# Kernel tuning notes

Hardware: AMD Instinct MI355X
Metric: run time of the kernel (lower is better)

The kernel has to match this reference:

```python
import jax, jax.numpy as jnp
import numpy as np

N_NODES = 60000
N_EDGES = 300000
FACE_DIM = 32
EDGE_DIM = 16
GF = 64   # EGAT node/edge hidden dim
EF = 32   # NNConv output dim
FF = 32   # placeholder point-transformer dim (zeros path)
TOT = GF + EF + FF  # 128
NEG_SLOPE = 0.01    # torch LeakyReLU default inside DGL EGATConv


def _leaky(x):
    return jnp.where(x >= 0, x, NEG_SLOPE * x)


def _edge_softmax(logits, dst, n):
    # softmax over incoming edges of each destination node (DGL edge_softmax)
    m = jax.ops.segment_max(logits, dst, num_segments=n)
    e = jnp.exp(logits - m[dst])
    s = jax.ops.segment_sum(e, dst, num_segments=n)
    return e / s[dst]


def _egat(h, f, src, dst, n, w_ni, w_nj, w_fij, w_node, attn, bias):
    # DGL EGATConv with num_heads=1 (head dim squeezed)
    f_out = _leaky((h @ w_ni)[src] + (h @ w_nj)[dst] + f @ w_fij + bias)  # (E, GF)
    a = _edge_softmax(f_out @ attn, dst, n)                               # (E,)
    msg = (h @ w_node)[src] * a[:, None]                                  # (E, GF)
    h_out = jax.ops.segment_sum(msg, dst, num_segments=n)                 # (N, GF)
    return h_out, f_out


def setup_inputs() -> dict:
    key = jax.random.key(0)
    ks = iter(jax.random.split(key, 40))

    def w(shape, scale=0.1):
        return jax.random.normal(next(ks), shape, dtype=jnp.float32) * scale

    inp = {
        "face_features": jax.random.normal(next(ks), (N_NODES, FACE_DIM), dtype=jnp.float32),
        "edge_features": jax.random.normal(next(ks), (N_EDGES, EDGE_DIM), dtype=jnp.float32),
        "fp_w": w((FACE_DIM, GF)), "fp_b": w((GF,)),
        "ep_w": w((EDGE_DIM, GF)), "ep_b": w((GF,)),
        "nn_w": w((EDGE_DIM, FACE_DIM * EF), 0.05), "nn_b": w((FACE_DIM * EF,), 0.05),
        "nn_bias": w((EF,)),
        "gate_w": w((TOT, 1)), "gate_b": w((1,)),
        "src": jax.random.randint(next(ks), (N_EDGES,), 0, N_NODES),
        "dst": jax.random.randint(next(ks), (N_EDGES,), 0, N_NODES),
    }
    for L in ("e1", "e2"):
        inp[f"{L}_ni"] = w((GF, GF))
        inp[f"{L}_nj"] = w((GF, GF))
        inp[f"{L}_fij"] = w((GF, GF))
        inp[f"{L}_node"] = w((GF, GF))
        inp[f"{L}_attn"] = w((GF,))
        inp[f"{L}_bias"] = w((GF,))
    return inp


def reference(face_features, edge_features, fp_w, fp_b, ep_w, ep_b,
              nn_w, nn_b, nn_bias, gate_w, gate_b,
              e1_ni, e1_nj, e1_fij, e1_node, e1_attn, e1_bias,
              e2_ni, e2_nj, e2_fij, e2_node, e2_attn, e2_bias,
              src, dst):
    n = face_features.shape[0]
    # --- Gf: two stacked EGATConv layers on projected features ---
    h = face_features @ fp_w + fp_b
    f = edge_features @ ep_w + ep_b
    h, f = _egat(h, f, src, dst, n, e1_ni, e1_nj, e1_fij, e1_node, e1_attn, e1_bias)
    h, f = _egat(h, f, src, dst, n, e2_ni, e2_nj, e2_fij, e2_node, e2_attn, e2_bias)
    Gf = h
    # --- Ef: NNConv (edge-conditioned conv, mean aggregation) ---
    W_e = (edge_features @ nn_w + nn_b).reshape(-1, FACE_DIM, EF)      # (E, 32, 32)
    m = jnp.einsum('ei,eio->eo', face_features[src], W_e)              # (E, EF)
    s = jax.ops.segment_sum(m, dst, num_segments=n)
    cnt = jax.ops.segment_sum(jnp.ones((m.shape[0],), m.dtype), dst, num_segments=n)
    Ef_feat = s / jnp.maximum(cnt, 1.0)[:, None] + nn_bias             # (N, EF)
    # --- Ff: zeros (face_point_features=None path) ---
    Ff_feat = jnp.zeros((n, FF), dtype=Gf.dtype)
    node_features = jnp.concatenate([Gf, Ef_feat, Ff_feat], axis=-1)   # (N, 128)
    # --- GlobalAttentionPooling (single graph) ---
    gate = jax.nn.softmax(node_features @ gate_w + gate_b, axis=0)     # (N, 1)
    graph_feat = jnp.sum(gate * node_features, axis=0, keepdims=True)  # (1, 128)
    return node_features, graph_feat
```

## Files before the change

### kernel.cpp

```cpp
#include <hip/hip_runtime.h>

#define NN 60000
#define NE 300000
#define PB 768
typedef unsigned short ush;
typedef __attribute__((ext_vector_type(8))) short bf16x8;
typedef __attribute__((ext_vector_type(4))) float f32x4;

static inline int cdiv(int a, int b) { return (a + b - 1) / b; }

__device__ inline unsigned ord_enc(float x) {
  unsigned u = __float_as_uint(x);
  return (u & 0x80000000u) ? ~u : (u | 0x80000000u);
}
__device__ inline float ord_dec(unsigned u) {
  return __uint_as_float((u & 0x80000000u) ? (u & 0x7fffffffu) : ~u);
}
__device__ inline float bf2f(unsigned u16) { return __uint_as_float(u16 << 16); }
__device__ inline ush f2bf(float x) {
  unsigned u = __float_as_uint(x);
  return (ush)((u + 0x7FFFu + ((u >> 16) & 1u)) >> 16);
}
__device__ inline unsigned pack2(float lo, float hi) {
  return ((unsigned)f2bf(hi) << 16) | (unsigned)f2bf(lo);
}

__global__ void deg_kernel(const int* __restrict__ key, int* __restrict__ deg) {
  int e = blockIdx.x * blockDim.x + threadIdx.x;
  if (e < NE) atomicAdd(deg + key[e], 1);
}

__global__ void scan1_kernel(const int* __restrict__ deg, int* __restrict__ rowptr,
                             int* __restrict__ partial) {
  __shared__ int s[256];
  int i = blockIdx.x * 256 + threadIdx.x;
  int v = (i < NN) ? deg[i] : 0;
  s[threadIdx.x] = v;
  __syncthreads();
  for (int off = 1; off < 256; off <<= 1) {
    int t = (threadIdx.x >= off) ? s[threadIdx.x - off] : 0;
    __syncthreads();
    s[threadIdx.x] += t;
    __syncthreads();
  }
  if (i < NN) rowptr[i] = s[threadIdx.x] - v;
  if (threadIdx.x == 255) partial[blockIdx.x] = s[255];
}

__global__ void scan2_kernel(int* __restrict__ partial, int nb) {
  __shared__ int s[256];
  int v = (threadIdx.x < nb) ? partial[threadIdx.x] : 0;
  s[threadIdx.x] = v;
  __syncthreads();
  for (int off = 1; off < 256; off <<= 1) {
    int t = (threadIdx.x >= off) ? s[threadIdx.x - off] : 0;
    __syncthreads();
    s[threadIdx.x] += t;
    __syncthreads();
  }
  if (threadIdx.x < nb) partial[threadIdx.x] = s[threadIdx.x] - v;
}

__global__ void scan3_kernel(int* __restrict__ rowptr, const int* __restrict__ partial,
                             int* __restrict__ cursor) {
  int i = blockIdx.x * 256 + threadIdx.x;
  if (i < NN) {
    int r = rowptr[i] + partial[blockIdx.x];
    rowptr[i] = r;
    cursor[i] = r;
  }
}

__global__ void scatter_dst_kernel(const int* __restrict__ src, const int* __restrict__ dst,
                                   const float* __restrict__ ef, int* __restrict__ cursor,
                                   int* __restrict__ src_s, int* __restrict__ dst_s,
                                   ush* __restrict__ ef16) {
  int e = blockIdx.x * blockDim.x + threadIdx.x;
  if (e >= NE) return;
  int d = dst[e];
  int j = atomicAdd(cursor + d, 1);
  src_s[j] = src[e];
  dst_s[j] = d;
  const float4* ep = (const float4*)(ef + (size_t)e * 16);
  float4 a = ep[0], b = ep[1], c = ep[2], dd = ep[3];
  uint4* bp = (uint4*)(ef16 + (size_t)j * 32);
  uint4 p0, p1;
  p0.x = pack2(a.x, a.y); p0.y = pack2(a.z, a.w);
  p0.z = pack2(b.x, b.y); p0.w = pack2(b.z, b.w);
  p1.x = pack2(c.x, c.y); p1.y = pack2(c.z, c.w);
  p1.z = pack2(dd.x, dd.y); p1.w = pack2(dd.z, dd.w);
  bp[0] = p0; bp[1] = p1;
  bp[2] = make_uint4(0, 0, 0, 0);
  bp[3] = make_uint4(0, 0, 0, 0);
}

__global__ void face16_kernel(const float* __restrict__ face, ush* __restrict__ face16) {
  int t = blockIdx.x * blockDim.x + threadIdx.x;
  if (t >= NN * 8) return;
  const float4 v = ((const float4*)face)[t];
  ((uint2*)face16)[t] = make_uint2(pack2(v.x, v.y), pack2(v.z, v.w));
}

__global__ void fold_kernel(const float* __restrict__ fp_w, const float* __restrict__ fp_b,
                            const float* __restrict__ ep_w, const float* __restrict__ ep_b,
                            const float* __restrict__ fij, const float* __restrict__ ebias,
                            const float* __restrict__ ni, const float* __restrict__ nj,
                            const float* __restrict__ node, float* __restrict__ fold) {
  int t = blockIdx.x * blockDim.x + threadIdx.x;
  if (t >= 7424) return;
  int o = t & 63;
  const float* A;
  const float* B;
  float init = 0.f;
  if (t < 1024)      { A = ep_w + (size_t)(t >> 6) * 64; B = fij + o; }
  else if (t < 1088) { A = ep_b; B = fij + o; init = ebias[o]; }
  else if (t < 3136) { A = fp_w + (size_t)((t - 1088) >> 6) * 64; B = ni + o; }
  else if (t < 5184) { A = fp_w + (size_t)((t - 3136) >> 6) * 64; B = nj + o; }
  else if (t < 7232) { A = fp_w + (size_t)((t - 5184) >> 6) * 64; B = node + o; }
  else if (t < 7296) { A = fp_b; B = ni + o; }
  else if (t < 7360) { A = fp_b; B = nj + o; }
  else               { A = fp_b; B = node + o; }
  float a = init;
  for (int i = 0; i < 64; ++i) a = fmaf(A[i], B[(size_t)i * 64], a);
  fold[t] = a;
}

__global__ void fold1_frag_kernel(const float* __restrict__ fold, ush* __restrict__ Wf1frag,
                                  ush* __restrict__ WfragH1) {
  int t = blockIdx.x * blockDim.x + threadIdx.x;
  if (t >= 2048 + 6144) return;
  if (t < 2048) {
    int i = t & 7, lane = (t >> 3) & 63, ct = t >> 9;
    int k = (lane >> 4) * 8 + i;
    int o = ct * 16 + (lane & 15);
    Wf1frag[t] = (k < 16) ? f2bf(fold[(size_t)k * 64 + o]) : 0;
  } else {
    int idx = t - 2048;
    int i = idx & 7, lane = (idx >> 3) & 63, ct = (idx >> 9) & 3, m = idx >> 11;
    int k = (lane >> 4) * 8 + i;
    int o = ct * 16 + (lane & 15);
    WfragH1[idx] = f2bf(fold[1088 + (size_t)m * 2048 + (size_t)k * 64 + o]);
  }
}

__global__ void nnwt_frag_kernel(const float* __restrict__ nn_w, const float* __restrict__ nn_b,
                                 ush* __restrict__ Wfrag) {
  int t = blockIdx.x * blockDim.x + threadIdx.x;
  if (t >= 17408) return;
  int i = t & 7, lane = (t >> 3) & 63, ct = (t >> 9) & 1, kk = t >> 10;
  int k = kk * 32 + (lane >> 4) * 8 + i;
  int o = ct * 16 + (lane & 15);
  float v = (k < 512) ? nn_w[(size_t)(k >> 5) * 1024 + (k & 31) * 32 + o]
                      : nn_b[(k - 512) * 32 + o];
  Wfrag[t] = f2bf(v);
}

__global__ void fij_frag_kernel(const float* __restrict__ fij, ush* __restrict__ Wfrag2) {
  int t = blockIdx.x * blockDim.x + threadIdx.x;
  if (t >= 4096) return;
  int i = t & 7, lane = (t >> 3) & 63, ct = (t >> 9) & 3, kk = t >> 11;
  int k = kk * 32 + (lane >> 4) * 8 + i;
  int o = ct * 16 + (lane & 15);
  Wfrag2[t] = f2bf(fij[(size_t)k * 64 + o]);
}

__global__ void hproj_frag_kernel(const float* __restrict__ ni, const float* __restrict__ nj,
                                  const float* __restrict__ node, ush* __restrict__ WfragH) {
  int t = blockIdx.x * blockDim.x + threadIdx.x;
  if (t >= 12288) return;
  int i = t & 7, lane = (t >> 3) & 63, ct = (t >> 9) & 3, kk = (t >> 11) & 1, m = t >> 12;
  int k = kk * 32 + (lane >> 4) * 8 + i;
  int o = ct * 16 + (lane & 15);
  const float* W = (m == 0) ? ni : (m == 1) ? nj : node;
  WfragH[t] = f2bf(W[(size_t)k * 64 + o]);
}

__global__ __launch_bounds__(256, 4) void mfma_hproj1_kernel(
    const ush* __restrict__ face16, const ush* __restrict__ WfragH1,
    const float* __restrict__ fold, ush* __restrict__ hs, ush* __restrict__ hd,
    ush* __restrict__ hn) {
  int wave = (blockIdx.x * blockDim.x + threadIdx.x) >> 6;
  int lane = threadIdx.x & 63;
  int m0 = wave * 16;
  if (m0 >= NN) return;
  int arow = lane & 15;
  int aoff = (lane >> 4) * 8;
  bf16x8 a = *(const bf16x8*)(face16 + (size_t)(m0 + arow) * 32 + aoff);
  int ccol = lane & 15;
  int crow = (lane >> 4) * 4;
#pragma unroll
  for (int m = 0; m < 3; ++m) {
    const ush* wm = WfragH1 + (size_t)m * 2048 + lane * 8;
    bf16x8 b0 = *(const bf16x8*)(wm + 0 * 512);
    bf16x8 b1 = *(const bf16x8*)(wm + 1 * 512);
    bf16x8 b2 = *(const bf16x8*)(wm + 2 * 512);
    bf16x8 b3 = *(const bf16x8*)(wm + 3 * 512);
    f32x4 acc0 = {0.f, 0.f, 0.f, 0.f};
    f32x4 acc1 = {0.f, 0.f, 0.f, 0.f};
    f32x4 acc2 = {0.f, 0.f, 0.f, 0.f};
    f32x4 acc3 = {0.f, 0.f, 0.f, 0.f};
    acc0 = __builtin_amdgcn_mfma_f32_16x16x32_bf16(a, b0, acc0, 0, 0, 0);
    acc1 = __builtin_amdgcn_mfma_f32_16x16x32_bf16(a, b1, acc1, 0, 0, 0);
    acc2 = __builtin_amdgcn_mfma_f32_16x16x32_bf16(a, b2, acc2, 0, 0, 0);
    acc3 = __builtin_amdgcn_mfma_f32_16x16x32_bf16(a, b3, acc3, 0, 0, 0);
    float bv0 = fold[7232 + m * 64 + ccol];
    float bv1 = fold[7232 + m * 64 + 16 + ccol];
    float bv2 = fold[7232 + m * 64 + 32 + ccol];
    float bv3 = fold[7232 + m * 64 + 48 + ccol];
    ush* outm = (m == 0) ? hs : (m == 1) ? hd : hn;
#pragma unroll
    for (int j = 0; j < 4; ++j) {
      ush* op = outm + (size_t)(m0 + crow + j) * 64;
      op[ccol] = f2bf(acc0[j] + bv0);
      op[16 + ccol] = f2bf(acc1[j] + bv1);
      op[32 + ccol] = f2bf(acc2[j] + bv2);
      op[48 + ccol] = f2bf(acc3[j] + bv3);
    }
  }
}

__global__ __launch_bounds__(256, 4) void mfma_fout1_kernel(
    const ush* __restrict__ ef16, const ush* __restrict__ Wf1frag, const float* __restrict__ fold,
    const ush* __restrict__ hs, const ush* __restrict__ hd, const int* __restrict__ src_s,
    const int* __restrict__ dst_s, const float* __restrict__ attn, ush* __restrict__ f116,
    float* __restrict__ logit) {
  int wave = (blockIdx.x * blockDim.x + threadIdx.x) >> 6;
  int lane = threadIdx.x & 63;
  int m0 = wave * 16;
  if (m0 >= NE) return;
  int arow = lane & 15;
  int aoff = (lane >> 4) * 8;
  bf16x8 a = *(const bf16x8*)(ef16 + (size_t)(m0 + arow) * 32 + aoff);
  const ush* wp = Wf1frag + lane * 8;
  bf16x8 b0 = *(const bf16x8*)(wp + 0 * 512);
  bf16x8 b1 = *(const bf16x8*)(wp + 1 * 512);
  bf16x8 b2 = *(const bf16x8*)(wp + 2 * 512);
  bf16x8 b3 = *(const bf16x8*)(wp + 3 * 512);
  f32x4 acc0 = {0.f, 0.f, 0.f, 0.f};
  f32x4 acc1 = {0.f, 0.f, 0.f, 0.f};
  f32x4 acc2 = {0.f, 0.f, 0.f, 0.f};
  f32x4 acc3 = {0.f, 0.f, 0.f, 0.f};
  acc0 = __builtin_amdgcn_mfma_f32_16x16x32_bf16(a, b0, acc0, 0, 0, 0);
  acc1 = __builtin_amdgcn_mfma_f32_16x16x32_bf16(a, b1, acc1, 0, 0, 0);
  acc2 = __builtin_amdgcn_mfma_f32_16x16x32_bf16(a, b2, acc2, 0, 0, 0);
  acc3 = __builtin_amdgcn_mfma_f32_16x16x32_bf16(a, b3, acc3, 0, 0, 0);
  int ccol = lane & 15;
  int crow = (lane >> 4) * 4;
  float av0 = attn[ccol], av1 = attn[16 + ccol], av2 = attn[32 + ccol], av3 = attn[48 + ccol];
  float bv0 = fold[1024 + ccol], bv1 = fold[1024 + 16 + ccol];
  float bv2 = fold[1024 + 32 + ccol], bv3 = fold[1024 + 48 + ccol];
#pragma unroll
  for (int j = 0; j < 4; ++j) {
    int r = m0 + crow + j;
    int s = src_s[r], d = dst_s[r];
    const ush* hsp = hs + (size_t)s * 64;
    const ush* hdp = hd + (size_t)d * 64;
    float f0 = acc0[j] + bf2f(hsp[ccol]) + bf2f(hdp[ccol]) + bv0;
    float f1 = acc1[j] + bf2f(hsp[16 + ccol]) + bf2f(hdp[16 + ccol]) + bv1;
    float f2 = acc2[j] + bf2f(hsp[32 + ccol]) + bf2f(hdp[32 + ccol]) + bv2;
    float f3 = acc3[j] + bf2f(hsp[48 + ccol]) + bf2f(hdp[48 + ccol]) + bv3;
    f0 = f0 >= 0.f ? f0 : 0.01f * f0;
    f1 = f1 >= 0.f ? f1 : 0.01f * f1;
    f2 = f2 >= 0.f ? f2 : 0.01f * f2;
    f3 = f3 >= 0.f ? f3 : 0.01f * f3;
    ush* fp = f116 + (size_t)r * 64;
    fp[ccol] = f2bf(f0);
    fp[16 + ccol] = f2bf(f1);
    fp[32 + ccol] = f2bf(f2);
    fp[48 + ccol] = f2bf(f3);
    float p = fmaf(f0, av0, fmaf(f1, av1, fmaf(f2, av2, f3 * av3)));
    p += __shfl_xor(p, 1, 64);
    p += __shfl_xor(p, 2, 64);
    p += __shfl_xor(p, 4, 64);
    p += __shfl_xor(p, 8, 64);
    if (ccol == 0) logit[r] = p;
  }
}

__global__ __launch_bounds__(256, 4) void mfma_hproj_kernel(
    const ush* __restrict__ h1bf, const ush* __restrict__ WfragH, ush* __restrict__ hs,
    ush* __restrict__ hd, ush* __restrict__ hn) {
  int wave = (blockIdx.x * blockDim.x + threadIdx.x) >> 6;
  int lane = threadIdx.x & 63;
  int m0 = wave * 16;
  if (m0 >= NN) return;
  int arow = lane & 15;
  int aoff = (lane >> 4) * 8;
  const ush* ap = h1bf + (size_t)(m0 + arow) * 64 + aoff;
  bf16x8 a0 = *(const bf16x8*)(ap);
  bf16x8 a1 = *(const bf16x8*)(ap + 32);
  const ush* wp = WfragH + lane * 8;
  int ccol = lane & 15;
  int crow = (lane >> 4) * 4;
#pragma unroll
  for (int m = 0; m < 3; ++m) {
    f32x4 acc0 = {0.f, 0.f, 0.f, 0.f};
    f32x4 acc1 = {0.f, 0.f, 0.f, 0.f};
    f32x4 acc2 = {0.f, 0.f, 0.f, 0.f};
    f32x4 acc3 = {0.f, 0.f, 0.f, 0.f};
    const ush* wm = wp + (size_t)m * 8 * 512;
    bf16x8 b0 = *(const bf16x8*)(wm + 0 * 512);
    bf16x8 b1 = *(const bf16x8*)(wm + 1 * 512);
    bf16x8 b2 = *(const bf16x8*)(wm + 2 * 512);
    bf16x8 b3 = *(const bf16x8*)(wm + 3 * 512);
    acc0 = __builtin_amdgcn_mfma_f32_16x16x32_bf16(a0, b0, acc0, 0, 0, 0);
    acc1 = __builtin_amdgcn_mfma_f32_16x16x32_bf16(a0, b1, acc1, 0, 0, 0);
    acc2 = __builtin_amdgcn_mfma_f32_16x16x32_bf16(a0, b2, acc2, 0, 0, 0);
    acc3 = __builtin_amdgcn_mfma_f32_16x16x32_bf16(a0, b3, acc3, 0, 0, 0);
    b0 = *(const bf16x8*)(wm + 4 * 512);
    b1 = *(const bf16x8*)(wm + 5 * 512);
    b2 = *(const bf16x8*)(wm + 6 * 512);
    b3 = *(const bf16x8*)(wm + 7 * 512);
    acc0 = __builtin_amdgcn_mfma_f32_16x16x32_bf16(a1, b0, acc0, 0, 0, 0);
    acc1 = __builtin_amdgcn_mfma_f32_16x16x32_bf16(a1, b1, acc1, 0, 0, 0);
    acc2 = __builtin_amdgcn_mfma_f32_16x16x32_bf16(a1, b2, acc2, 0, 0, 0);
    acc3 = __builtin_amdgcn_mfma_f32_16x16x32_bf16(a1, b3, acc3, 0, 0, 0);
    ush* outm = (m == 0) ? hs : (m == 1) ? hd : hn;
#pragma unroll
    for (int j = 0; j < 4; ++j) {
      ush* op = outm + (size_t)(m0 + crow + j) * 64;
      op[ccol] = f2bf(acc0[j]);
      op[16 + ccol] = f2bf(acc1[j]);
      op[32 + ccol] = f2bf(acc2[j]);
      op[48 + ccol] = f2bf(acc3[j]);
    }
  }
}

__global__ __launch_bounds__(256, 4) void mfma_fout_kernel(
    const ush* __restrict__ f116, const ush* __restrict__ Wfrag2, const float* __restrict__ bias,
    const ush* __restrict__ hs, const ush* __restrict__ hd, const int* __restrict__ src_s,
    const int* __restrict__ dst_s, const float* __restrict__ attn, float* __restrict__ logit) {
  int wave = (blockIdx.x * blockDim.x + threadIdx.x) >> 6;
  int lane = threadIdx.x & 63;
  int m0 = wave * 16;
  if (m0 >= NE) return;
  int arow = lane & 15;
  int aoff = (lane >> 4) * 8;
  const ush* ap = f116 + (size_t)(m0 + arow) * 64 + aoff;
  const ush* wp = Wfrag2 + lane * 8;
  f32x4 acc0 = {0.f, 0.f, 0.f, 0.f};
  f32x4 acc1 = {0.f, 0.f, 0.f, 0.f};
  f32x4 acc2 = {0.f, 0.f, 0.f, 0.f};
  f32x4 acc3 = {0.f, 0.f, 0.f, 0.f};
#pragma unroll
  for (int kk = 0; kk < 2; ++kk) {
    bf16x8 a = *(const bf16x8*)(ap + kk * 32);
    bf16x8 b0 = *(const bf16x8*)(wp + (size_t)(kk * 4 + 0) * 512);
    bf16x8 b1 = *(const bf16x8*)(wp + (size_t)(kk * 4 + 1) * 512);
    bf16x8 b2 = *(const bf16x8*)(wp + (size_t)(kk * 4 + 2) * 512);
    bf16x8 b3 = *(const bf16x8*)(wp + (size_t)(kk * 4 + 3) * 512);
    acc0 = __builtin_amdgcn_mfma_f32_16x16x32_bf16(a, b0, acc0, 0, 0, 0);
    acc1 = __builtin_amdgcn_mfma_f32_16x16x32_bf16(a, b1, acc1, 0, 0, 0);
    acc2 = __builtin_amdgcn_mfma_f32_16x16x32_bf16(a, b2, acc2, 0, 0, 0);
    acc3 = __builtin_amdgcn_mfma_f32_16x16x32_bf16(a, b3, acc3, 0, 0, 0);
  }
  int ccol = lane & 15;
  int crow = (lane >> 4) * 4;
  float av0 = attn[ccol], av1 = attn[16 + ccol], av2 = attn[32 + ccol], av3 = attn[48 + ccol];
  float bv0 = bias[ccol], bv1 = bias[16 + ccol], bv2 = bias[32 + ccol], bv3 = bias[48 + ccol];
#pragma unroll
  for (int j = 0; j < 4; ++j) {
    int r = m0 + crow + j;
    int s = src_s[r], d = dst_s[r];
    const ush* hsp = hs + (size_t)s * 64;
    const ush* hdp = hd + (size_t)d * 64;
    float f0 = acc0[j] + bf2f(hsp[ccol]) + bf2f(hdp[ccol]) + bv0;
    float f1 = acc1[j] + bf2f(hsp[16 + ccol]) + bf2f(hdp[16 + ccol]) + bv1;
    float f2 = acc2[j] + bf2f(hsp[32 + ccol]) + bf2f(hdp[32 + ccol]) + bv2;
    float f3 = acc3[j] + bf2f(hsp[48 + ccol]) + bf2f(hdp[48 + ccol]) + bv3;
    f0 = f0 >= 0.f ? f0 : 0.01f * f0;
    f1 = f1 >= 0.f ? f1 : 0.01f * f1;
    f2 = f2 >= 0.f ? f2 : 0.01f * f2;
    f3 = f3 >= 0.f ? f3 : 0.01f * f3;
    float p = fmaf(f0, av0, fmaf(f1, av1, fmaf(f2, av2, f3 * av3)));
    p += __shfl_xor(p, 1, 64);
    p += __shfl_xor(p, 2, 64);
    p += __shfl_xor(p, 4, 64);
    p += __shfl_xor(p, 8, 64);
    if (ccol == 0) logit[r] = p;
  }
}

template <bool BF16OUT>
__global__ __launch_bounds__(256, 4) void agg_gather_kernel(
    const ush* __restrict__ hn, const float* __restrict__ logit, const int* __restrict__ rowptr,
    const int* __restrict__ deg, const int* __restrict__ src_s, void* __restrict__ hnew) {
  int wave = (blockIdx.x * blockDim.x + threadIdx.x) >> 6;
  int lane = threadIdx.x & 63;
  if (wave >= NN) return;
  int n = wave, d = deg[n], r0 = rowptr[n];
  if (d == 0) {
    if (BF16OUT) ((ush*)hnew)[(size_t)n * 64 + lane] = 0;
    else ((float*)hnew)[(size_t)n * 64 + lane] = 0.f;
    return;
  }
  float sum = 0.f, acc0 = 0.f, acc1 = 0.f, acc2 = 0.f, acc3 = 0.f;
  int j = 0;
  for (; j + 3 < d; j += 4) {
    int jj = r0 + j;
    int s0 = src_s[jj + 0], s1 = src_s[jj + 1], s2 = src_s[jj + 2], s3 = src_s[jj + 3];
    float l0 = logit[jj + 0], l1 = logit[jj + 1], l2 = logit[jj + 2], l3 = logit[jj + 3];
    ush h0 = hn[(size_t)s0 * 64 + lane];
    ush h1 = hn[(size_t)s1 * 64 + lane];
    ush h2 = hn[(size_t)s2 * 64 + lane];
    ush h3 = hn[(size_t)s3 * 64 + lane];
    float w0 = __expf(l0), w1 = __expf(l1);
    float w2 = __expf(l2), w3 = __expf(l3);
    sum += (w0 + w1) + (w2 + w3);
    acc0 = fmaf(w0, bf2f(h0), acc0);
    acc1 = fmaf(w1, bf2f(h1), acc1);
    acc2 = fmaf(w2, bf2f(h2), acc2);
    acc3 = fmaf(w3, bf2f(h3), acc3);
  }
  for (; j < d; ++j) {
    int jj = r0 + j;
    float w = __expf(logit[jj]);
    sum += w;
    acc0 = fmaf(w, bf2f(hn[(size_t)src_s[jj] * 64 + lane]), acc0);
  }
  float r = ((acc0 + acc1) + (acc2 + acc3)) / sum;
  if (BF16OUT) ((ush*)hnew)[(size_t)n * 64 + lane] = f2bf(r);
  else ((float*)hnew)[(size_t)n * 64 + lane] = r;
}

__global__ __launch_bounds__(256, 4) void nnconv_G_kernel(
    const float* __restrict__ face, const ush* __restrict__ ef16,
    const int* __restrict__ rowptr, const int* __restrict__ deg, const int* __restrict__ src_s,
    ush* __restrict__ G) {
  int wave = (blockIdx.x * blockDim.x + threadIdx.x) >> 6;
  int lane = threadIdx.x & 63;
  if (wave >= NN) return;
  int n = wave, d = deg[n], r0 = rowptr[n];
  int k4 = lane >> 2, ib = lane & 3;
  float g[8], fs[8];
#pragma unroll
  for (int u = 0; u < 8; ++u) { g[u] = 0.f; fs[u] = 0.f; }
  int j = 0;
  for (; j + 1 < d; j += 2) {
    int jj = r0 + j;
    int s0 = src_s[jj], s1 = src_s[jj + 1];
    float ev0 = bf2f(ef16[(size_t)jj * 32 + k4]);
    float ev1 = bf2f(ef16[(size_t)(jj + 1) * 32 + k4]);
    const float4* fp0 = (const float4*)(face + (size_t)s0 * 32 + ib * 8);
    const float4* fp1 = (const float4*)(face + (size_t)s1 * 32 + ib * 8);
    float4 fa0 = fp0[0], fb0 = fp0[1];
    float4 fa1 = fp1[0], fb1 = fp1[1];
    g[0] = fmaf(ev0, fa0.x, g[0]); g[1] = fmaf(ev0, fa0.y, g[1]);
    g[2] = fmaf(ev0, fa0.z, g[2]); g[3] = fmaf(ev0, fa0.w, g[3]);
    g[4] = fmaf(ev0, fb0.x, g[4]); g[5] = fmaf(ev0, fb0.y, g[5]);
    g[6] = fmaf(ev0, fb0.z, g[6]); g[7] = fmaf(ev0, fb0.w, g[7]);
    g[0] = fmaf(ev1, fa1.x, g[0]); g[1] = fmaf(ev1, fa1.y, g[1]);
    g[2] = fmaf(ev1, fa1.z, g[2]); g[3] = fmaf(ev1, fa1.w, g[3]);
    g[4] = fmaf(ev1, fb1.x, g[4]); g[5] = fmaf(ev1, fb1.y, g[5]);
    g[6] = fmaf(ev1, fb1.z, g[6]); g[7] = fmaf(ev1, fb1.w, g[7]);
    if (k4 == 0) {
      fs[0] += fa0.x + fa1.x; fs[1] += fa0.y + fa1.y;
      fs[2] += fa0.z + fa1.z; fs[3] += fa0.w + fa1.w;
      fs[4] += fb0.x + fb1.x; fs[5] += fb0.y + fb1.y;
      fs[6] += fb0.z + fb1.z; fs[7] += fb0.w + fb1.w;
    }
  }
  if (j < d) {
    int jj = r0 + j;
    int s0 = src_s[jj];
    float ev0 = bf2f(ef16[(size_t)jj * 32 + k4]);
    const float4* fp0 = (const float4*)(face + (size_t)s0 * 32 + ib * 8);
    float4 fa0 = fp0[0], fb0 = fp0[1];
    g[0] = fmaf(ev0, fa0.x, g[0]); g[1] = fmaf(ev0, fa0.y, g[1]);
    g[2] = fmaf(ev0, fa0.z, g[2]); g[3] = fmaf(ev0, fa0.w, g[3]);
    g[4] = fmaf(ev0, fb0.x, g[4]); g[5] = fmaf(ev0, fb0.y, g[5]);
    g[6] = fmaf(ev0, fb0.z, g[6]); g[7] = fmaf(ev0, fb0.w, g[7]);
    if (k4 == 0) {
      fs[0] += fa0.x; fs[1] += fa0.y; fs[2] += fa0.z; fs[3] += fa0.w;
      fs[4] += fb0.x; fs[5] += fb0.y; fs[6] += fb0.z; fs[7] += fb0.w;
    }
  }
  uint4 pv;
  pv.x = pack2(g[0], g[1]); pv.y = pack2(g[2], g[3]);
  pv.z = pack2(g[4], g[5]); pv.w = pack2(g[6], g[7]);
  *(uint4*)(G + (size_t)n * 544 + lane * 8) = pv;
  if (k4 == 0) {
    uint4 fv;
    fv.x = pack2(fs[0], fs[1]); fv.y = pack2(fs[2], fs[3]);
    fv.z = pack2(fs[4], fs[5]); fv.w = pack2(fs[6], fs[7]);
    *(uint4*)(G + (size_t)n * 544 + 512 + ib * 8) = fv;
  }
}

__global__ __launch_bounds__(256, 4) void gemm_G_mfma_kernel(const ush* __restrict__ G,
                                                             const ush* __restrict__ Wfrag,
                                                             float* __restrict__ sArr,
                                                             int rows) {
  int wave = (blockIdx.x * blockDim.x + threadIdx.x) >> 6;
  int lane = threadIdx.x & 63;
  int m0 = wave * 16;
  if (m0 >= rows) return;
  int arow = lane & 15;
  int aoff = (lane >> 4) * 8;
  const ush* gp = G + (size_t)(m0 + arow) * 544 + aoff;
  const ush* wp = Wfrag + lane * 8;
  f32x4 acc0 = {0.f, 0.f, 0.f, 0.f};
  f32x4 acc1 = {0.f, 0.f, 0.f, 0.f};
#pragma unroll 4
  for (int kk = 0; kk < 17; ++kk) {
    bf16x8 a = *(const bf16x8*)(gp + kk * 32);
    bf16x8 b0 = *(const bf16x8*)(wp + (size_t)(kk * 2 + 0) * 512);
    bf16x8 b1 = *(const bf16x8*)(wp + (size_t)(kk * 2 + 1) * 512);
    acc0 = __builtin_amdgcn_mfma_f32_16x16x32_bf16(a, b0, acc0, 0, 0, 0);
    acc1 = __builtin_amdgcn_mfma_f32_16x16x32_bf16(a, b1, acc1, 0, 0, 0);
  }
  int ccol = lane & 15;
  int crow = (lane >> 4) * 4;
#pragma unroll
  for (int j = 0; j < 4; ++j) {
    int r = m0 + crow + j;
    sArr[(size_t)r * 32 + ccol] = acc0[j];
    sArr[(size_t)r * 32 + 16 + ccol] = acc1[j];
  }
}

__global__ void combine_gate_kernel(const float* __restrict__ hfin, const float* __restrict__ sArr,
                                    const int* __restrict__ deg, const float* __restrict__ nn_bias,
                                    const float* __restrict__ gate_w, const float* __restrict__ gate_b,
                                    float* __restrict__ out, float* __restrict__ g) {
  int wave = (blockIdx.x * blockDim.x + threadIdx.x) >> 6;
  int lane = threadIdx.x & 63;
  if (wave >= NN) return;
  int n = wave;
  float v0 = hfin[(size_t)n * 64 + lane];
  int c1 = lane + 64;
  float v1 = (c1 < 96)
                 ? sArr[(size_t)n * 32 + (c1 - 64)] / fmaxf((float)deg[n], 1.0f) + nn_bias[c1 - 64]
                 : 0.f;
  out[(size_t)n * 128 + lane] = v0;
  out[(size_t)n * 128 + c1] = v1;
  float p = v0 * gate_w[lane] + ((c1 < 96) ? v1 * gate_w[c1] : 0.f);
#pragma unroll
  for (int off = 32; off; off >>= 1) p += __shfl_xor(p, off, 64);
  if (lane == 0) g[n] = p + gate_b[0];
}

__global__ void gate_max_kernel(const float* __restrict__ g, unsigned* __restrict__ gmax) {
  int tid = blockIdx.x * blockDim.x + threadIdx.x;
  int stride = gridDim.x * blockDim.x;
  float v = -3.0e38f;
  for (int n = tid; n < NN; n += stride) v = fmaxf(v, g[n]);
#pragma unroll
  for (int off = 32; off; off >>= 1) v = fmaxf(v, __shfl_xor(v, off, 64));
  __shared__ float sm[4];
  int lane = threadIdx.x & 63, wid = threadIdx.x >> 6;
  if (lane == 0) sm[wid] = v;
  __syncthreads();
  if (threadIdx.x == 0) {
    float m = fmaxf(fmaxf(sm[0], sm[1]), fmaxf(sm[2], sm[3]));
    atomicMax(gmax, ord_enc(m));
  }
}

__global__ __launch_bounds__(256, 4) void pool_exp_kernel(
    const float* __restrict__ nf, const float* __restrict__ g, const unsigned* __restrict__ gmax,
    float* __restrict__ pacc, float* __restrict__ wsb) {
  int o = threadIdx.x & 127;
  int half = threadIdx.x >> 7;
  int ri = blockIdx.x * 2 + half;
  float m = ord_dec(*gmax);
  float acc0 = 0.f, acc1 = 0.f, ws = 0.f;
  int n = ri;
  const int STR = PB * 2;
  for (; n + STR < NN; n += STR * 2) {
    float w0 = __expf(g[n] - m);
    float w1 = __expf(g[n + STR] - m);
    float v0 = nf[(size_t)n * 128 + o];
    float v1 = nf[(size_t)(n + STR) * 128 + o];
    ws += w0 + w1;
    acc0 = fmaf(w0, v0, acc0);
    acc1 = fmaf(w1, v1, acc1);
  }
  if (n < NN) {
    float w = __expf(g[n] - m);
    ws += w;
    acc0 = fmaf(w, nf[(size_t)n * 128 + o], acc0);
  }
  pacc[(size_t)ri * 128 + o] = acc0 + acc1;
  if (o == 0) wsb[ri] = ws;
}

__global__ void pool_reduce_kernel(const float* __restrict__ pacc, const float* __restrict__ wsb,
                                   float* __restrict__ gacc, float* __restrict__ gsum) {
  int b = blockIdx.x;
  int t = threadIdx.x;
  float v = 0.f;
  if (b < 128) {
    for (int ri = t; ri < PB * 2; ri += 256) v += pacc[(size_t)ri * 128 + b];
  } else {
    for (int ri = t; ri < PB * 2; ri += 256) v += wsb[ri];
  }
#pragma unroll
  for (int off = 32; off; off >>= 1) v += __shfl_xor(v, off, 64);
  __shared__ float sm[4];
  int lane = t & 63, wid = t >> 6;
  if (lane == 0) sm[wid] = v;
  __syncthreads();
  if (t == 0) {
    float s = (sm[0] + sm[1]) + (sm[2] + sm[3]);
    if (b < 128) gacc[b] = s;
    else gsum[0] = s;
  }
}

__global__ void finalize_kernel(const float* __restrict__ gacc, const float* __restrict__ gsum,
                                float* __restrict__ out) {
  int o = threadIdx.x;
  if (o < 128) out[(size_t)NN * 128 + o] = gacc[o] / gsum[0];
}

extern "C" void kernel_launch(void* const* d_in, const int* in_sizes, int n_in,
                              void* d_out, int out_size, void* d_ws, size_t ws_size,
                              hipStream_t stream) {
  const float* face    = (const float*)d_in[0];
  const float* ef      = (const float*)d_in[1];
  const float* fp_w    = (const float*)d_in[2];
  const float* fp_b    = (const float*)d_in[3];
  const float* ep_w    = (const float*)d_in[4];
  const float* ep_b    = (const float*)d_in[5];
  const float* nn_w    = (const float*)d_in[6];
  const float* nn_b    = (const float*)d_in[7];
  const float* nn_bias = (const float*)d_in[8];
  const float* gate_w  = (const float*)d_in[9];
  const float* gate_b  = (const float*)d_in[10];
  const int*   src     = (const int*)d_in[11];
  const int*   dst     = (const int*)d_in[12];
  const float* e1_attn = (const float*)d_in[17];
  const float* e2_ni   = (const float*)d_in[19];
  const float* e2_nj   = (const float*)d_in[20];
  const float* e2_fij  = (const float*)d_in[21];
  const float* e2_attn = (const float*)d_in[23];
  const float* e2_bias = (const float*)d_in[24];
  float* out = (float*)d_out;

  char* p = (char*)d_ws;
  auto alloc = [&](size_t nfloats) {
    float* r = (float*)p;
    p += ((nfloats * 4 + 255) / 256) * 256;
    return r;
  };
  float* h0 = alloc((size_t)NN * 64);
  ush* h1bf = (ush*)alloc((size_t)NN * 32);
  char* bigreg = p;
  ush* hs16 = (ush*)alloc((size_t)NN * 32);
  ush* hd16 = (ush*)alloc((size_t)NN * 32);
  ush* hn16 = (ush*)alloc((size_t)NN * 32);
  ush* f116 = (ush*)alloc((size_t)NE * 32);
  float* logit = alloc(NE);
  {
    size_t used = (size_t)(p - bigreg);
    size_t need = (size_t)NN * 544 * 2;
    if (used < need) p += ((need - used + 255) / 256) * 256;
  }
  ush* G = (ush*)bigreg;
  float* sArr  = alloc((size_t)NN * 32);
  float* g     = alloc(NN);
  float* gacc  = alloc(128);
  float* gsum  = alloc(1);
  unsigned* gmax = (unsigned*)alloc(1);
  float* fold  = alloc(7424);
  ush* Wfrag   = (ush*)alloc(17408 / 2);
  ush* Wfrag2  = (ush*)alloc(4096 / 2);
  ush* WfragH  = (ush*)alloc(12288 / 2);
  ush* Wf1frag = (ush*)alloc(2048 / 2);
  ush* WfragH1 = (ush*)alloc(6144 / 2);
  ush* face16  = (ush*)alloc((size_t)NN * 16);
  ush* ef16    = (ush*)alloc((size_t)NE * 16);
  float* pacc  = alloc((size_t)PB * 2 * 128);
  float* wsb   = alloc(PB * 2);
  int* deg    = (int*)alloc(NN);
  int* rowptr = (int*)alloc(NN);
  int* cursor = (int*)alloc(NN);
  int* partial = (int*)alloc(256);
  int* src_s  = (int*)alloc(NE);
  int* dst_s  = (int*)alloc(NE);

  const int B = 256;
  const int NB256 = cdiv(NN, 256);

  hipMemsetAsync(deg, 0, NN * 4, stream);
  deg_kernel<<<cdiv(NE, B), B, 0, stream>>>(dst, deg);
  scan1_kernel<<<NB256, 256, 0, stream>>>(deg, rowptr, partial);
  scan2_kernel<<<1, 256, 0, stream>>>(partial, NB256);
  scan3_kernel<<<NB256, 256, 0, stream>>>(rowptr, partial, cursor);
  scatter_dst_kernel<<<cdiv(NE, B), B, 0, stream>>>(src, dst, ef, cursor, src_s, dst_s, ef16);

  fold_kernel<<<29, B, 0, stream>>>(fp_w, fp_b, ep_w, ep_b,
                                    (const float*)d_in[15], (const float*)d_in[18],
                                    (const float*)d_in[13], (const float*)d_in[14],
                                    (const float*)d_in[16], fold);
  fold1_frag_kernel<<<32, B, 0, stream>>>(fold, Wf1frag, WfragH1);
  nnwt_frag_kernel<<<68, B, 0, stream>>>(nn_w, nn_b, Wfrag);
  fij_frag_kernel<<<16, B, 0, stream>>>(e2_fij, Wfrag2);
  hproj_frag_kernel<<<48, B, 0, stream>>>(e2_ni, e2_nj, (const float*)d_in[22], WfragH);
  face16_kernel<<<cdiv(NN * 8, B), B, 0, stream>>>(face, face16);

  mfma_hproj1_kernel<<<cdiv(NN * 4, B), B, 0, stream>>>(face16, WfragH1, fold, hs16, hd16, hn16);
  mfma_fout1_kernel<<<cdiv(NE * 4, B), B, 0, stream>>>(ef16, Wf1frag, fold, hs16, hd16,
                                                       src_s, dst_s, e1_attn, f116, logit);
  agg_gather_kernel<true><<<cdiv(NN * 64, B), B, 0, stream>>>(hn16, logit, rowptr, deg,
                                                              src_s, h1bf);

  mfma_hproj_kernel<<<cdiv(NN * 4, B), B, 0, stream>>>(h1bf, WfragH, hs16, hd16, hn16);
  mfma_fout_kernel<<<cdiv(NE * 4, B), B, 0, stream>>>(f116, Wfrag2, e2_bias, hs16, hd16,
                                                      src_s, dst_s, e2_attn, logit);
  agg_gather_kernel<false><<<cdiv(NN * 64, B), B, 0, stream>>>(hn16, logit, rowptr, deg,
                                                               src_s, h0);

  nnconv_G_kernel<<<cdiv(NN * 64, B), B, 0, stream>>>(face, ef16, rowptr, deg, src_s, G);
  gemm_G_mfma_kernel<<<cdiv(NN * 4, B), B, 0, stream>>>(G, Wfrag, sArr, NN);

  hipMemsetAsync(gmax, 0, 4, stream);
  combine_gate_kernel<<<cdiv(NN * 64, B), B, 0, stream>>>(h0, sArr, deg, nn_bias, gate_w,
                                                          gate_b, out, g);
  gate_max_kernel<<<128, B, 0, stream>>>(g, gmax);
  pool_exp_kernel<<<PB, B, 0, stream>>>(out, g, gmax, pacc, wsb);
  pool_reduce_kernel<<<129, B, 0, stream>>>(pacc, wsb, gacc, gsum);
  finalize_kernel<<<1, 128, 0, stream>>>(gacc, gsum, out);
}
```

Before: 255.5 us.

## Fuse NNConv gather and MFMA GEMM via shared-memory G tile

Merges the NNConv edge-gather kernel and the following MFMA GEMM into one kernel. Each block builds a 16-row G tile in LDS and then runs the GEMM from it, so the large G intermediate in global memory (about 65 MB) is neither written nor read back. Face features are now read as bf16 instead of fp32, which halves gather bytes but lowers input precision. Each wave now processes 4 nodes one after another, and only 2 of the 4 waves run the MFMA stage, so there is less parallelism to hide gather latency.

After: 241.2 us. 1.06x faster.

```diff
diff --git a/kernel.cpp b/kernel.cpp
--- a/kernel.cpp
+++ b/kernel.cpp
@@ -23,6 +23,12 @@
 }
 __device__ inline unsigned pack2(float lo, float hi) {
   return ((unsigned)f2bf(hi) << 16) | (unsigned)f2bf(lo);
+}
+__device__ inline void unp8(uint4 u, float* f) {
+  f[0] = bf2f(u.x & 0xffff); f[1] = bf2f(u.x >> 16);
+  f[2] = bf2f(u.y & 0xffff); f[3] = bf2f(u.y >> 16);
+  f[4] = bf2f(u.z & 0xffff); f[5] = bf2f(u.z >> 16);
+  f[6] = bf2f(u.w & 0xffff); f[7] = bf2f(u.w >> 16);
 }
 
 __global__ void deg_kernel(const int* __restrict__ key, int* __restrict__ deg) {
@@ -424,99 +430,87 @@
   else ((float*)hnew)[(size_t)n * 64 + lane] = r;
 }
 
-__global__ __launch_bounds__(256, 4) void nnconv_G_kernel(
-    const float* __restrict__ face, const ush* __restrict__ ef16,
-    const int* __restrict__ rowptr, const int* __restrict__ deg, const int* __restrict__ src_s,
-    ush* __restrict__ G) {
-  int wave = (blockIdx.x * blockDim.x + threadIdx.x) >> 6;
+__global__ __launch_bounds__(256, 4) void nnconv_fused_kernel(
+    const ush* __restrict__ face16, const ush* __restrict__ ef16,
+    const int* __restrict__ rowptr, const int* __restrict__ deg,
+    const int* __restrict__ src_s, const ush* __restrict__ Wfrag,
+    float* __restrict__ sArr) {
+  __shared__ ush Gs[16][552];
+  int wid = threadIdx.x >> 6;
   int lane = threadIdx.x & 63;
-  if (wave >= NN) return;
-  int n = wave, d = deg[n], r0 = rowptr[n];
+  int nbase = blockIdx.x * 16;
   int k4 = lane >> 2, ib = lane & 3;
-  float g[8], fs[8];
-#pragma unroll
-  for (int u = 0; u < 8; ++u) { g[u] = 0.f; fs[u] = 0.f; }
-  int j = 0;
-  for (; j + 1 < d; j += 2) {
-    int jj = r0 + j;
-    int s0 = src_s[jj], s1 = src_s[jj + 1];
-    float ev0 = bf2f(ef16[(size_t)jj * 32 + k4]);
-    float ev1 = bf2f(ef16[(size_t)(jj + 1) * 32 + k4]);
-    const float4* fp0 = (const float4*)(face + (size_t)s0 * 32 + ib * 8);
-    const float4* fp1 = (const float4*)(face + (size_t)s1 * 32 + ib * 8);
-    float4 fa0 = fp0[0], fb0 = fp0[1];
-    float4 fa1 = fp1[0], fb1 = fp1[1];
-    g[0] = fmaf(ev0, fa0.x, g[0]); g[1] = fmaf(ev0, fa0.y, g[1]);
-    g[2] = fmaf(ev0, fa0.z, g[2]); g[3] = fmaf(ev0, fa0.w, g[3]);
-    g[4] = fmaf(ev0, fb0.x, g[4]); g[5] = fmaf(ev0, fb0.y, g[5]);
-    g[6] = fmaf(ev0, fb0.z, g[6]); g[7] = fmaf(ev0, fb0.w, g[7]);
-    g[0] = fmaf(ev1, fa1.x, g[0]); g[1] = fmaf(ev1, fa1.y, g[1]);
-    g[2] = fmaf(ev1, fa1.z, g[2]); g[3] = fmaf(ev1, fa1.w, g[3]);
-    g[4] = fmaf(ev1, fb1.x, g[4]); g[5] = fmaf(ev1, fb1.y, g[5]);
-    g[6] = fmaf(ev1, fb1.z, g[6]); g[7] = fmaf(ev1, fb1.w, g[7]);
+  for (int q = 0; q < 4; ++q) {
+    int row = wid * 4 + q;
+    int n = nbase + row;
+    int d = deg[n], r0 = rowptr[n];
+    float g[8], fs[8];
+#pragma unroll
+    for (int u = 0; u < 8; ++u) { g[u] = 0.f; fs[u] = 0.f; }
+    int j = 0;
+    for (; j + 1 < d; j += 2) {
+      int jj = r0 + j;
+      int s0 = src_s[jj], s1 = src_s[jj + 1];
+      float ev0 = bf2f(ef16[(size_t)jj * 32 + k4]);
+      float ev1 = bf2f(ef16[(size_t)(jj + 1) * 32 + k4]);
+      uint4 u0 = *(const uint4*)(face16 + (size_t)s0 * 32 + ib * 8);
+      uint4 u1 = *(const uint4*)(face16 + (size_t)s1 * 32 + ib * 8);
+      float fa0[8], fa1[8];
+      unp8(u0, fa0);
+      unp8(u1, fa1);
+#pragma unroll
+      for (int u = 0; u < 8; ++u) {
+        g[u] = fmaf(ev0, fa0[u], g[u]);
+        g[u] = fmaf(ev1, fa1[u], g[u]);
+      }
+      if (k4 == 0) {
+#pragma unroll
+        for (int u = 0; u < 8; ++u) fs[u] += fa0[u] + fa1[u];
+      }
+    }
+    if (j < d) {
+      int jj = r0 + j;
+      float ev0 = bf2f(ef16[(size_t)jj * 32 + k4]);
+      uint4 u0 = *(const uint4*)(face16 + (size_t)src_s[jj] * 32 + ib * 8);
+      float fa0[8];
+      unp8(u0, fa0);
+#pragma unroll
+      for (int u = 0; u < 8; ++u) g[u] = fmaf(ev0, fa0[u], g[u]);
+      if (k4 == 0) {
+#pragma unroll
+        for (int u = 0; u < 8; ++u) fs[u] += fa0[u];
+      }
+    }
+    uint4 pv;
+    pv.x = pack2(g[0], g[1]); pv.y = pack2(g[2], g[3]);
+    pv.z = pack2(g[4], g[5]); pv.w = pack2(g[6], g[7]);
+    *(uint4*)&Gs[row][lane * 8] = pv;
     if (k4 == 0) {
-      fs[0] += fa0.x + fa1.x; fs[1] += fa0.y + fa1.y;
-      fs[2] += fa0.z + fa1.z; fs[3] += fa0.w + fa1.w;
-      fs[4] += fb0.x + fb1.x; fs[5] += fb0.y + fb1.y;
-      fs[6] += fb0.z + fb1.z; fs[7] += fb0.w + fb1.w;
+      uint4 fv;
+      fv.x = pack2(fs[0], fs[1]); fv.y = pack2(fs[2], fs[3]);
+      fv.z = pack2(fs[4], fs[5]); fv.w = pack2(fs[6], fs[7]);
+      *(uint4*)&Gs[row][512 + ib * 8] = fv;
     }
   }
-  if (j < d) {
-    int jj = r0 + j;
-    int s0 = src_s[jj];
-    float ev0 = bf2f(ef16[(size_t)jj * 32 + k4]);
-    const float4* fp0 = (const float4*)(face + (size_t)s0 * 32 + ib * 8);
-    float4 fa0 = fp0[0], fb0 = fp0[1];
-    g[0] = fmaf(ev0, fa0.x, g[0]); g[1] = fmaf(ev0, fa0.y, g[1]);
-    g[2] = fmaf(ev0, fa0.z, g[2]); g[3] = fmaf(ev0, fa0.w, g[3]);
-    g[4] = fmaf(ev0, fb0.x, g[4]); g[5] = fmaf(ev0, fb0.y, g[5]);
-    g[6] = fmaf(ev0, fb0.z, g[6]); g[7] = fmaf(ev0, fb0.w, g[7]);
-    if (k4 == 0) {
-      fs[0] += fa0.x; fs[1] += fa0.y; fs[2] += fa0.z; fs[3] += fa0.w;
-      fs[4] += fb0.x; fs[5] += fb0.y; fs[6] += fb0.z; fs[7] += fb0.w;
+  __syncthreads();
+  if (wid < 2) {
+    int arow = lane & 15;
+    int aoff = (lane >> 4) * 8;
+    const ush* wp = Wfrag + lane * 8;
+    f32x4 acc = {0.f, 0.f, 0.f, 0.f};
+#pragma unroll 4
+    for (int kk = 0; kk < 17; ++kk) {
+      bf16x8 a = *(const bf16x8*)&Gs[arow][kk * 32 + aoff];
+      bf16x8 b = *(const bf16x8*)(wp + (size_t)(kk * 2 + wid) * 512);
+      acc = __builtin_amdgcn_mfma_f32_16x16x32_bf16(a, b, acc, 0, 0, 0);
     }
-  }
-  uint4 pv;
-  pv.x = pack2(g[0], g[1]); pv.y = pack2(g[2], g[3]);
-  pv.z = pack2(g[4], g[5]); pv.w = pack2(g[6], g[7]);
-  *(uint4*)(G + (size_t)n * 544 + lane * 8) = pv;
-  if (k4 == 0) {
-    uint4 fv;
-    fv.x = pack2(fs[0], fs[1]); fv.y = pack2(fs[2], fs[3]);
-    fv.z = pack2(fs[4], fs[5]); fv.w = pack2(fs[6], fs[7]);
-    *(uint4*)(G + (size_t)n * 544 + 512 + ib * 8) = fv;
-  }
-}
-
-__global__ __launch_bounds__(256, 4) void gemm_G_mfma_kernel(const ush* __restrict__ G,
-                                                             const ush* __restrict__ Wfrag,
-                                                             float* __restrict__ sArr,
-                                                             int rows) {
-  int wave = (blockIdx.x * blockDim.x + threadIdx.x) >> 6;
-  int lane = threadIdx.x & 63;
-  int m0 = wave * 16;
-  if (m0 >= rows) return;
-  int arow = lane & 15;
-  int aoff = (lane >> 4) * 8;
-  const ush* gp = G + (size_t)(m0 + arow) * 544 + aoff;
-  const ush* wp = Wfrag + lane * 8;
-  f32x4 acc0 = {0.f, 0.f, 0.f, 0.f};
-  f32x4 acc1 = {0.f, 0.f, 0.f, 0.f};
-#pragma unroll 4
-  for (int kk = 0; kk < 17; ++kk) {
-    bf16x8 a = *(const bf16x8*)(gp + kk * 32);
-    bf16x8 b0 = *(const bf16x8*)(wp + (size_t)(kk * 2 + 0) * 512);
-    bf16x8 b1 = *(const bf16x8*)(wp + (size_t)(kk * 2 + 1) * 512);
-    acc0 = __builtin_amdgcn_mfma_f32_16x16x32_bf16(a, b0, acc0, 0, 0, 0);
-    acc1 = __builtin_amdgcn_mfma_f32_16x16x32_bf16(a, b1, acc1, 0, 0, 0);
-  }
-  int ccol = lane & 15;
-  int crow = (lane >> 4) * 4;
-#pragma unroll
-  for (int j = 0; j < 4; ++j) {
-    int r = m0 + crow + j;
-    sArr[(size_t)r * 32 + ccol] = acc0[j];
-    sArr[(size_t)r * 32 + 16 + ccol] = acc1[j];
+    int ccol = lane & 15;
+    int crow = (lane >> 4) * 4;
+#pragma unroll
+    for (int j = 0; j < 4; ++j) {
+      int r = nbase + crow + j;
+      sArr[(size_t)r * 32 + wid * 16 + ccol] = acc[j];
+    }
   }
 }
 
@@ -647,18 +641,11 @@
   };
   float* h0 = alloc((size_t)NN * 64);
   ush* h1bf = (ush*)alloc((size_t)NN * 32);
-  char* bigreg = p;
   ush* hs16 = (ush*)alloc((size_t)NN * 32);
   ush* hd16 = (ush*)alloc((size_t)NN * 32);
   ush* hn16 = (ush*)alloc((size_t)NN * 32);
   ush* f116 = (ush*)alloc((size_t)NE * 32);
   float* logit = alloc(NE);
-  {
-    size_t used = (size_t)(p - bigreg);
-    size_t need = (size_t)NN * 544 * 2;
-    if (used < need) p += ((need - used + 255) / 256) * 256;
-  }
-  ush* G = (ush*)bigreg;
   float* sArr  = alloc((size_t)NN * 32);
   float* g     = alloc(NN);
   float* gacc  = alloc(128);
@@ -713,8 +700,7 @@
   agg_gather_kernel<false><<<cdiv(NN * 64, B), B, 0, stream>>>(hn16, logit, rowptr, deg,
                                                                src_s, h0);
 
-  nnconv_G_kernel<<<cdiv(NN * 64, B), B, 0, stream>>>(face, ef16, rowptr, deg, src_s, G);
-  gemm_G_mfma_kernel<<<cdiv(NN * 4, B), B, 0, stream>>>(G, Wfrag, sArr, NN);
+  nnconv_fused_kernel<<<NN / 16, B, 0, stream>>>(face16, ef16, rowptr, deg, src_s, Wfrag, sArr);
 
   hipMemsetAsync(gmax, 0, 4, stream);
   combine_gate_kernel<<<cdiv(NN * 64, B), B, 0, stream>>>(h0, sArr, deg, nn_bias, gate_w,
```
